# Optimization experiments

Measured on AMD Instinct MI355X. Metric: run time of the kernel, lower is better.

Reference implementation:

```python
import jax, jax.numpy as jnp
import numpy as np

N = 262144
D = 128
E = 524288
N_PHYS = 5
EPS_SL = 1e-8
EPS_LN = 1e-5


def _signed_log(x):
    return jnp.sign(x) * jnp.log(jnp.abs(x) + EPS_SL)


def setup_inputs() -> dict:
    key = jax.random.key(0)
    ks = jax.random.split(key, 12)
    h = jax.random.normal(ks[0], (N, D), dtype=jnp.float32)
    c1 = jax.random.normal(ks[1], (N,), dtype=jnp.float32)
    c2 = jax.random.normal(ks[2], (N,), dtype=jnp.float32)
    c3 = jax.random.normal(ks[3], (N,), dtype=jnp.float32)
    c4 = jax.random.normal(ks[4], (N,), dtype=jnp.float32)
    q_new = jax.random.normal(ks[5], (N,), dtype=jnp.float32)
    src = jax.random.randint(ks[6], (E,), 0, N, dtype=jnp.int64)
    dst = jax.random.randint(ks[7], (E,), 0, N, dtype=jnp.int64)
    d_in = 2 * D + N_PHYS
    W1 = jax.random.normal(ks[8], (d_in, D), dtype=jnp.float32) / np.sqrt(d_in)
    b1 = jnp.zeros((D,), dtype=jnp.float32)
    W2 = jax.random.normal(ks[9], (D, D), dtype=jnp.float32) / np.sqrt(D)
    b2 = jnp.zeros((D,), dtype=jnp.float32)
    gamma = jnp.ones((D,), dtype=jnp.float32)
    beta = jnp.zeros((D,), dtype=jnp.float32)
    return {"h": h, "c1_next_upstream": c1, "c2_prev_upstream": c2,
            "c3_self": c3, "c4_lateral": c4, "q_new": q_new,
            "src": src, "dst": dst,
            "W1": W1, "b1": b1, "W2": W2, "b2": b2,
            "gamma": gamma, "beta": beta}


def reference(h, c1_next_upstream, c2_prev_upstream, c3_self, c4_lateral,
              q_new, src, dst, W1, b1, W2, b2, gamma, beta):
    # sparse adjacency matmul: upstream_h[i] = sum_{j: j->i} h[j]
    upstream_h = jax.ops.segment_sum(h[src], dst, num_segments=h.shape[0])
    phys = jnp.stack([_signed_log(c1_next_upstream),
                      _signed_log(c2_prev_upstream),
                      _signed_log(c3_self),
                      _signed_log(c4_lateral),
                      _signed_log(q_new)], axis=-1)  # (N, 5)
    node_input = jnp.concatenate([h, upstream_h, phys], axis=-1)  # (N, 2D+5)
    hid = jax.nn.silu(node_input @ W1 + b1)
    mlp_out = hid @ W2 + b2
    z = h + mlp_out
    mean = jnp.mean(z, axis=-1, keepdims=True)
    var = jnp.var(z, axis=-1, keepdims=True)
    return (z - mean) * jax.lax.rsqrt(var + EPS_LN) * gamma + beta
```

## Files before the change

kernel.cpp:

```cpp
#include <hip/hip_runtime.h>
#include <math.h>

#define NN 262144
#define DD 128
#define EPS_SL 1e-8f
#define EPS_LN 1e-5f
#define THREADS 512
#define TILE_M 64
#define NBLOCKS 256
#define NTILES (NN / TILE_M)
#define TPB (NTILES / NBLOCKS)

typedef __attribute__((ext_vector_type(8))) short bf16x8;
typedef __attribute__((ext_vector_type(4))) float f32x4;

#define OFF_W1 0
#define OFF_W2 73728
#define OFF_X  106496
#define OFF_H  143360
#define OFF_RED 159744
#define SMEM_TOT 161792

#define WS_OFFS   0
#define WS_CURSOR 1048832
#define WS_BSUM   2097408
#define WS_ESRC   2101504
#define WS_NEEDED (2101504 + 524288 * 4)

__device__ inline unsigned short f2bf(float f) {
    union { float f; unsigned int i; } v; v.f = f;
    unsigned int r = v.i + 0x7fffu + ((v.i >> 16) & 1u);
    return (unsigned short)(r >> 16);
}
__device__ inline unsigned int pack2(float a, float b) {
    return (unsigned int)f2bf(a) | ((unsigned int)f2bf(b) << 16);
}
__device__ inline uint4 pack8(float4 a, float4 b) {
    return make_uint4(pack2(a.x, a.y), pack2(a.z, a.w),
                      pack2(b.x, b.y), pack2(b.z, b.w));
}
__device__ inline float signed_log(float x) {
    float l = __logf(fabsf(x) + EPS_SL);
    return (x > 0.f) ? l : ((x < 0.f) ? -l : 0.f);
}
__device__ inline void stx(unsigned short* sX, int kb, int row, uint4 v) {
    *(uint4*)(sX + (((kb * 64 + row) ^ (kb & 7)) * 8)) = v;
}
__device__ inline bf16x8 ldx(const unsigned short* sX, int kb, int row) {
    return *(const bf16x8*)(sX + (((kb * 64 + row) ^ (kb & 7)) * 8));
}

__global__ void hist_kernel(const int* __restrict__ dst, int* counts, int E) {
    int e = blockIdx.x * blockDim.x + threadIdx.x;
    if (e < E) atomicAdd(&counts[dst[e]], 1);
}

__global__ void scan_local(int* offs, int* bsum) {
    __shared__ int tmp[256];
    int t = threadIdx.x, i = blockIdx.x * 256 + t;
    int own = offs[i];
    tmp[t] = own;
    __syncthreads();
    for (int off = 1; off < 256; off <<= 1) {
        int v = (t >= off) ? tmp[t - off] : 0;
        __syncthreads();
        tmp[t] += v;
        __syncthreads();
    }
    offs[i] = tmp[t] - own;
    if (t == 255) bsum[blockIdx.x] = tmp[255];
}

__global__ void scan_bsum(int* bsum) {
    __shared__ int tmp[1024];
    int t = threadIdx.x;
    int own = bsum[t];
    tmp[t] = own;
    __syncthreads();
    for (int off = 1; off < 1024; off <<= 1) {
        int v = (t >= off) ? tmp[t - off] : 0;
        __syncthreads();
        tmp[t] += v;
        __syncthreads();
    }
    bsum[t] = tmp[t] - own;
}

__global__ void scan_fixup(int* offs, const int* __restrict__ bsum, int* cursor, int E) {
    int i = blockIdx.x * 256 + threadIdx.x;
    int v = offs[i] + bsum[i >> 8];
    offs[i] = v;
    cursor[i] = v;
    if (i == 0) offs[NN] = E;
}

__global__ void fill_kernel(const int* __restrict__ src, const int* __restrict__ dst,
                            int* cursor, int* esrc, int E) {
    int e = blockIdx.x * blockDim.x + threadIdx.x;
    if (e < E) {
        int p = atomicAdd(&cursor[dst[e]], 1);
        esrc[p] = src[e];
    }
}

__global__ __launch_bounds__(256) void gather_kernel(
    const float4* __restrict__ h4, const int* __restrict__ offs,
    const int* __restrict__ esrc, char* outb)
{
    int stride = gridDim.x * 256;
    for (int idx = blockIdx.x * 256 + threadIdx.x; idx < NN * 16; idx += stride) {
        int n = idx >> 4, c = idx & 15;
        int o0 = offs[n], o1 = offs[n + 1];
        float4 a = make_float4(0.f, 0.f, 0.f, 0.f);
        float4 b = make_float4(0.f, 0.f, 0.f, 0.f);
        for (int e = o0; e < o1; ++e) {
            const float4* hr = h4 + (size_t)esrc[e] * 32 + c * 2;
            float4 p0 = hr[0], p1 = hr[1];
            a.x += p0.x; a.y += p0.y; a.z += p0.z; a.w += p0.w;
            b.x += p1.x; b.y += p1.y; b.z += p1.z; b.w += p1.w;
        }
        *(uint4*)(outb + (size_t)n * 512 + c * 16) = pack8(a, b);
    }
}

__global__ void scatter_kernel(const float4* __restrict__ h4,
                               const int* __restrict__ src,
                               const int* __restrict__ dst,
                               float* up, int E) {
    int tid = blockIdx.x * blockDim.x + threadIdx.x;
    int e = tid >> 5;
    if (e >= E) return;
    int c = tid & 31;
    float4 v = h4[(size_t)src[e] * 32 + c];
    float* o = up + (size_t)dst[e] * DD + c * 4;
    atomicAdd(o + 0, v.x);
    atomicAdd(o + 1, v.y);
    atomicAdd(o + 2, v.z);
    atomicAdd(o + 3, v.w);
}

template <int GATHER>
__global__ __launch_bounds__(THREADS) void node_kernel(
    const float* __restrict__ h, const void* up,
    const float* __restrict__ c1, const float* __restrict__ c2,
    const float* __restrict__ c3, const float* __restrict__ c4,
    const float* __restrict__ qn,
    const float* __restrict__ W1, const float* __restrict__ b1,
    const float* __restrict__ W2, const float* __restrict__ b2,
    const float* __restrict__ gamma, const float* __restrict__ beta,
    float* out)
{
    extern __shared__ char smem[];
    unsigned short* sW1 = (unsigned short*)(smem + OFF_W1);
    unsigned short* sW2 = (unsigned short*)(smem + OFF_W2);
    unsigned short* sX  = (unsigned short*)(smem + OFF_X);
    unsigned short* sH  = (unsigned short*)(smem + OFF_H);
    float2* red = (float2*)(smem + OFF_RED);

    const int tid = threadIdx.x;

    for (int c = tid; c < 36 * 128; c += THREADS) {
        int kb = c >> 7, n = c & 127;
        unsigned short tmp[8] __attribute__((aligned(16)));
        #pragma unroll
        for (int j = 0; j < 8; ++j) {
            int k = kb * 8 + j;
            tmp[j] = (k < 261) ? f2bf(W1[k * DD + n]) : (unsigned short)0;
        }
        *(uint4*)(sW1 + c * 8) = *(const uint4*)tmp;
    }
    for (int c = tid; c < 16 * 128; c += THREADS) {
        int kb = c >> 7, n = c & 127;
        unsigned short tmp[8] __attribute__((aligned(16)));
        #pragma unroll
        for (int j = 0; j < 8; ++j) tmp[j] = f2bf(W2[(kb * 8 + j) * DD + n]);
        *(uint4*)(sW2 + c * 8) = *(const uint4*)tmp;
    }
    if (tid < 192) {
        int kb = 33 + (tid >> 6), row = tid & 63;
        stx(sX, kb, row, make_uint4(0u, 0u, 0u, 0u));
    }

    const int lane = tid & 63;
    const int w    = tid >> 6;
    const int wm   = w >> 2;
    const int wn   = w & 3;
    const int l15  = lane & 15;
    const int lk   = lane >> 4;
    const int col0 = wn * 32 + l15;
    const int col1 = col0 + 16;

    const float b1v[2] = {b1[col0], b1[col1]};
    const float b2v[2] = {b2[col0], b2[col1]};
    const float gv[2]  = {gamma[col0], gamma[col1]};
    const float bv[2]  = {beta[col0], beta[col1]};

    const bf16x8* W1f = (const bf16x8*)sW1;
    const bf16x8* Hf  = (const bf16x8*)sH;
    const bf16x8* W2f = (const bf16x8*)sW2;

    const int k0 = tid & 15;
    const int r0 = tid >> 4;

    float4 h0a, h0b, h1a, h1b;
    uint4  u0, u1;
    float4 v0a, v0b, v1a, v1b;
    float pc1 = 0.f, pc2 = 0.f, pc3 = 0.f, pc4 = 0.f, pc5 = 0.f;

    {
        int base = blockIdx.x * TPB * TILE_M;
        const float* hp = h + (size_t)(base + r0) * DD + k0 * 8;
        h0a = *(const float4*)hp;       h0b = *(const float4*)(hp + 4);
        h1a = *(const float4*)(hp + 32 * DD); h1b = *(const float4*)(hp + 32 * DD + 4);
        if (GATHER) {
            const char* ub = (const char*)up;
            u0 = *(const uint4*)(ub + (size_t)(base + r0) * 512 + k0 * 16);
            u1 = *(const uint4*)(ub + (size_t)(base + r0 + 32) * 512 + k0 * 16);
        } else {
            const float* uf = (const float*)up + (size_t)(base + r0) * DD + k0 * 8;
            v0a = *(const float4*)uf;       v0b = *(const float4*)(uf + 4);
            v1a = *(const float4*)(uf + 32 * DD); v1b = *(const float4*)(uf + 32 * DD + 4);
        }
        if (tid < 64) {
            int n0 = base + tid;
            pc1 = c1[n0]; pc2 = c2[n0]; pc3 = c3[n0]; pc4 = c4[n0]; pc5 = qn[n0];
        }
    }
    __syncthreads();

    for (int tt = 0; tt < TPB; ++tt) {
        const int base = (blockIdx.x * TPB + tt) * TILE_M;

        stx(sX, k0, r0,      pack8(h0a, h0b));
        stx(sX, k0, r0 + 32, pack8(h1a, h1b));
        if (GATHER) {
            stx(sX, 16 + k0, r0,      u0);
            stx(sX, 16 + k0, r0 + 32, u1);
        } else {
            stx(sX, 16 + k0, r0,      pack8(v0a, v0b));
            stx(sX, 16 + k0, r0 + 32, pack8(v1a, v1b));
        }
        if (tid < 64) {
            uint4 pv = make_uint4(pack2(signed_log(pc1), signed_log(pc2)),
                                  pack2(signed_log(pc3), signed_log(pc4)),
                                  pack2(signed_log(pc5), 0.f), 0u);
            stx(sX, 32, tid, pv);
        }

        if (tt + 1 < TPB) {
            int bn = base + TILE_M;
            const float* hp = h + (size_t)(bn + r0) * DD + k0 * 8;
            h0a = *(const float4*)hp;       h0b = *(const float4*)(hp + 4);
            h1a = *(const float4*)(hp + 32 * DD); h1b = *(const float4*)(hp + 32 * DD + 4);
            if (GATHER) {
                const char* ub = (const char*)up;
                u0 = *(const uint4*)(ub + (size_t)(bn + r0) * 512 + k0 * 16);
                u1 = *(const uint4*)(ub + (size_t)(bn + r0 + 32) * 512 + k0 * 16);
            } else {
                const float* uf = (const float*)up + (size_t)(bn + r0) * DD + k0 * 8;
                v0a = *(const float4*)uf;       v0b = *(const float4*)(uf + 4);
                v1a = *(const float4*)(uf + 32 * DD); v1b = *(const float4*)(uf + 32 * DD + 4);
            }
            if (tid < 64) {
                int n0 = bn + tid;
                pc1 = c1[n0]; pc2 = c2[n0]; pc3 = c3[n0]; pc4 = c4[n0]; pc5 = qn[n0];
            }
        }
        __syncthreads();

        f32x4 acc[2][2] = {};
        #pragma unroll
        for (int ks = 0; ks < 9; ++ks) {
            int kb = ks * 4 + lk;
            bf16x8 a0  = ldx(sX, kb, wm * 32 + l15);
            bf16x8 a1  = ldx(sX, kb, wm * 32 + 16 + l15);
            bf16x8 bb0 = W1f[kb * 128 + col0];
            bf16x8 bb1 = W1f[kb * 128 + col1];
            acc[0][0] = __builtin_amdgcn_mfma_f32_16x16x32_bf16(a0, bb0, acc[0][0], 0, 0, 0);
            acc[0][1] = __builtin_amdgcn_mfma_f32_16x16x32_bf16(a0, bb1, acc[0][1], 0, 0, 0);
            acc[1][0] = __builtin_amdgcn_mfma_f32_16x16x32_bf16(a1, bb0, acc[1][0], 0, 0, 0);
            acc[1][1] = __builtin_amdgcn_mfma_f32_16x16x32_bf16(a1, bb1, acc[1][1], 0, 0, 0);
        }
        #pragma unroll
        for (int fm = 0; fm < 2; ++fm) {
            int row = wm * 32 + fm * 16 + lk * 4;
            #pragma unroll
            for (int fn = 0; fn < 2; ++fn) {
                int col = wn * 32 + fn * 16 + l15;
                int kbh = col >> 3, ko = col & 7;
                #pragma unroll
                for (int r = 0; r < 4; ++r) {
                    float v = acc[fm][fn][r] + b1v[fn];
                    float sg = 1.f / (1.f + __expf(-v));
                    sH[(kbh * 64 + row + r) * 8 + ko] = f2bf(v * sg);
                }
            }
        }
        __syncthreads();

        f32x4 acc2[2][2] = {};
        #pragma unroll
        for (int ks = 0; ks < 4; ++ks) {
            int kb = ks * 4 + lk;
            bf16x8 a0  = Hf[kb * 64 + wm * 32 + l15];
            bf16x8 a1  = Hf[kb * 64 + wm * 32 + 16 + l15];
            bf16x8 bb0 = W2f[kb * 128 + col0];
            bf16x8 bb1 = W2f[kb * 128 + col1];
            acc2[0][0] = __builtin_amdgcn_mfma_f32_16x16x32_bf16(a0, bb0, acc2[0][0], 0, 0, 0);
            acc2[0][1] = __builtin_amdgcn_mfma_f32_16x16x32_bf16(a0, bb1, acc2[0][1], 0, 0, 0);
            acc2[1][0] = __builtin_amdgcn_mfma_f32_16x16x32_bf16(a1, bb0, acc2[1][0], 0, 0, 0);
            acc2[1][1] = __builtin_amdgcn_mfma_f32_16x16x32_bf16(a1, bb1, acc2[1][1], 0, 0, 0);
        }

        float rs1[2][4], rs2[2][4];
        #pragma unroll
        for (int fm = 0; fm < 2; ++fm) {
            #pragma unroll
            for (int r = 0; r < 4; ++r) {
                size_t rowg = (size_t)(base + wm * 32 + fm * 16 + lk * 4 + r) * DD;
                float z0 = acc2[fm][0][r] + b2v[0] + h[rowg + col0];
                float z1 = acc2[fm][1][r] + b2v[1] + h[rowg + col1];
                acc2[fm][0][r] = z0; acc2[fm][1][r] = z1;
                float s = z0 + z1, q = z0 * z0 + z1 * z1;
                #pragma unroll
                for (int off = 1; off < 16; off <<= 1) {
                    s += __shfl_xor(s, off);
                    q += __shfl_xor(q, off);
                }
                rs1[fm][r] = s; rs2[fm][r] = q;
            }
        }
        if (l15 == 0) {
            #pragma unroll
            for (int fm = 0; fm < 2; ++fm)
                #pragma unroll
                for (int r = 0; r < 4; ++r)
                    red[wn * 64 + wm * 32 + fm * 16 + lk * 4 + r] =
                        make_float2(rs1[fm][r], rs2[fm][r]);
        }
        __syncthreads();

        #pragma unroll
        for (int fm = 0; fm < 2; ++fm) {
            #pragma unroll
            for (int r = 0; r < 4; ++r) {
                int rloc = wm * 32 + fm * 16 + lk * 4 + r;
                float2 t0 = red[rloc], t1 = red[64 + rloc],
                       t2 = red[128 + rloc], t3 = red[192 + rloc];
                float S = t0.x + t1.x + t2.x + t3.x;
                float Q = t0.y + t1.y + t2.y + t3.y;
                float mean = S * (1.f / 128.f);
                float var  = Q * (1.f / 128.f) - mean * mean;
                float rstd = rsqrtf(var + EPS_LN);
                size_t rowg = (size_t)(base + rloc) * DD;
                out[rowg + col0] = (acc2[fm][0][r] - mean) * rstd * gv[0] + bv[0];
                out[rowg + col1] = (acc2[fm][1][r] - mean) * rstd * gv[1] + bv[1];
            }
        }
    }
}

extern "C" void kernel_launch(void* const* d_in, const int* in_sizes, int n_in,
                              void* d_out, int out_size, void* d_ws, size_t ws_size,
                              hipStream_t stream) {
    const float* h     = (const float*)d_in[0];
    const float* c1    = (const float*)d_in[1];
    const float* c2    = (const float*)d_in[2];
    const float* c3    = (const float*)d_in[3];
    const float* c4    = (const float*)d_in[4];
    const float* qn    = (const float*)d_in[5];
    const int*   src   = (const int*)d_in[6];
    const int*   dst   = (const int*)d_in[7];
    const float* W1    = (const float*)d_in[8];
    const float* b1    = (const float*)d_in[9];
    const float* W2    = (const float*)d_in[10];
    const float* b2    = (const float*)d_in[11];
    const float* gamma = (const float*)d_in[12];
    const float* beta  = (const float*)d_in[13];
    float* out = (float*)d_out;
    int E = in_sizes[6];

    if (ws_size >= (size_t)WS_NEEDED) {
        char* ws = (char*)d_ws;
        int* offs   = (int*)(ws + WS_OFFS);
        int* cursor = (int*)(ws + WS_CURSOR);
        int* bsum   = (int*)(ws + WS_BSUM);
        int* esrc   = (int*)(ws + WS_ESRC);

        hipMemsetAsync(offs, 0, (size_t)NN * sizeof(int), stream);
        int eb = (E + 255) / 256;
        hist_kernel<<<eb, 256, 0, stream>>>(dst, offs, E);
        scan_local<<<NN / 256, 256, 0, stream>>>(offs, bsum);
        scan_bsum<<<1, 1024, 0, stream>>>(bsum);
        scan_fixup<<<NN / 256, 256, 0, stream>>>(offs, bsum, cursor, E);
        fill_kernel<<<eb, 256, 0, stream>>>(src, dst, cursor, esrc, E);

        gather_kernel<<<2048, 256, 0, stream>>>((const float4*)h, offs, esrc, (char*)d_out);

        hipFuncSetAttribute(reinterpret_cast<const void*>(&node_kernel<1>),
                            hipFuncAttributeMaxDynamicSharedMemorySize, SMEM_TOT);
        node_kernel<1><<<NBLOCKS, THREADS, SMEM_TOT, stream>>>(
            h, d_out, c1, c2, c3, c4, qn,
            W1, b1, W2, b2, gamma, beta, out);
    } else {
        hipMemsetAsync(d_out, 0, (size_t)NN * DD * sizeof(float), stream);
        int sthreads = E * 32;
        int sblocks = (sthreads + 255) / 256;
        scatter_kernel<<<sblocks, 256, 0, stream>>>((const float4*)h, src, dst, out, E);
        hipFuncSetAttribute(reinterpret_cast<const void*>(&node_kernel<0>),
                            hipFuncAttributeMaxDynamicSharedMemorySize, SMEM_TOT);
        node_kernel<0><<<NBLOCKS, THREADS, SMEM_TOT, stream>>>(
            h, d_out, c1, c2, c3, c4, qn,
            W1, b1, W2, b2, gamma, beta, out);
    }
}
```

Measured before the change: 232.6 us.

## Pack h with gathered sums in bf16 slots and rewrite node kernel per-wave

The gather kernel now also writes h itself as bf16 into the second half of each 512-byte output slot, so the node kernel reads one contiguous bf16 row per node instead of separate fp32 h and upstream buffers. The node kernel is restructured so that each wave independently handles 16-row strips. It uses transposed MFMA operands, a per-wave LDS hidden buffer and shuffle-based LayerNorm, which removes block-wide syncs and the staged X tile. The W1 rows are permuted to match the new slot order. The residual add now uses the bf16-rounded copy of h, which reduces precision slightly.

```diff
diff --git a/kernel.cpp b/kernel.cpp
--- a/kernel.cpp
+++ b/kernel.cpp
@@ -6,32 +6,37 @@
 #define EPS_SL 1e-8f
 #define EPS_LN 1e-5f
 #define THREADS 512
-#define TILE_M 64
 #define NBLOCKS 256
-#define NTILES (NN / TILE_M)
-#define TPB (NTILES / NBLOCKS)
 
 typedef __attribute__((ext_vector_type(8))) short bf16x8;
 typedef __attribute__((ext_vector_type(4))) float f32x4;
 
-#define OFF_W1 0
-#define OFF_W2 73728
-#define OFF_X  106496
-#define OFF_H  143360
-#define OFF_RED 159744
-#define SMEM_TOT 161792
+#define OFF_W1  0
+#define OFF_W2  73728
+#define OFF_B   106496
+#define OFF_HID 108544
+#define SMEM_TOT 141312
+
+#define FB_OFF_W1 0
+#define FB_OFF_W2 73728
+#define FB_OFF_X  106496
+#define FB_OFF_H  143360
+#define FB_OFF_RED 159744
+#define FB_SMEM_TOT 161792
 
 #define WS_OFFS   0
 #define WS_CURSOR 1048832
 #define WS_BSUM   2097408
 #define WS_ESRC   2101504
-#define WS_NEEDED (2101504 + 524288 * 4)
 
 __device__ inline unsigned short f2bf(float f) {
     union { float f; unsigned int i; } v; v.f = f;
     unsigned int r = v.i + 0x7fffu + ((v.i >> 16) & 1u);
     return (unsigned short)(r >> 16);
 }
+__device__ inline float bf2f(unsigned short u) {
+    union { float f; unsigned int i; } v; v.i = ((unsigned int)u) << 16; return v.f;
+}
 __device__ inline unsigned int pack2(float a, float b) {
     return (unsigned int)f2bf(a) | ((unsigned int)f2bf(b) << 16);
 }
@@ -43,10 +48,10 @@
     float l = __logf(fabsf(x) + EPS_SL);
     return (x > 0.f) ? l : ((x < 0.f) ? -l : 0.f);
 }
-__device__ inline void stx(unsigned short* sX, int kb, int row, uint4 v) {
+__device__ inline void stx64(unsigned short* sX, int kb, int row, uint4 v) {
     *(uint4*)(sX + (((kb * 64 + row) ^ (kb & 7)) * 8)) = v;
 }
-__device__ inline bf16x8 ldx(const unsigned short* sX, int kb, int row) {
+__device__ inline bf16x8 ldx64(const unsigned short* sX, int kb, int row) {
     return *(const bf16x8*)(sX + (((kb * 64 + row) ^ (kb & 7)) * 8));
 }
 
@@ -119,7 +124,11 @@
             a.x += p0.x; a.y += p0.y; a.z += p0.z; a.w += p0.w;
             b.x += p1.x; b.y += p1.y; b.z += p1.z; b.w += p1.w;
         }
-        *(uint4*)(outb + (size_t)n * 512 + c * 16) = pack8(a, b);
+        const float4* hn = h4 + (size_t)n * 32 + c * 2;
+        float4 q0 = hn[0], q1 = hn[1];
+        char* slot = outb + (size_t)n * 512;
+        *(uint4*)(slot + c * 16)       = pack8(a, b);
+        *(uint4*)(slot + 256 + c * 16) = pack8(q0, q1);
     }
 }
 
@@ -139,9 +148,8 @@
     atomicAdd(o + 3, v.w);
 }
 
-template <int GATHER>
-__global__ __launch_bounds__(THREADS) void node_kernel(
-    const float* __restrict__ h, const void* up,
+__global__ __launch_bounds__(THREADS, 2) void node_kernel(
+    const void* slots,
     const float* __restrict__ c1, const float* __restrict__ c2,
     const float* __restrict__ c3, const float* __restrict__ c4,
     const float* __restrict__ qn,
@@ -153,19 +161,24 @@
     extern __shared__ char smem[];
     unsigned short* sW1 = (unsigned short*)(smem + OFF_W1);
     unsigned short* sW2 = (unsigned short*)(smem + OFF_W2);
-    unsigned short* sX  = (unsigned short*)(smem + OFF_X);
-    unsigned short* sH  = (unsigned short*)(smem + OFF_H);
-    float2* red = (float2*)(smem + OFF_RED);
-
-    const int tid = threadIdx.x;
+    float* sB = (float*)(smem + OFF_B);
+
+    const int tid  = threadIdx.x;
+    const int lane = tid & 63;
+    const int wv   = tid >> 6;
+    const int m    = lane & 15;
+    const int lk   = lane >> 4;
+    unsigned short* sHid = (unsigned short*)(smem + OFF_HID + wv * 4096);
+    const int hswz = (m & 3) << 5;
 
     for (int c = tid; c < 36 * 128; c += THREADS) {
         int kb = c >> 7, n = c & 127;
         unsigned short tmp[8] __attribute__((aligned(16)));
         #pragma unroll
         for (int j = 0; j < 8; ++j) {
-            int k = kb * 8 + j;
-            tmp[j] = (k < 261) ? f2bf(W1[k * DD + n]) : (unsigned short)0;
+            int kx = kb * 8 + j;
+            int krow = (kx < 128) ? (128 + kx) : (kx < 256 ? kx - 128 : kx);
+            tmp[j] = (krow < 261) ? f2bf(W1[krow * DD + n]) : (unsigned short)0;
         }
         *(uint4*)(sW1 + c * 8) = *(const uint4*)tmp;
     }
@@ -176,9 +189,151 @@
         for (int j = 0; j < 8; ++j) tmp[j] = f2bf(W2[(kb * 8 + j) * DD + n]);
         *(uint4*)(sW2 + c * 8) = *(const uint4*)tmp;
     }
+    if (tid < 128) {
+        sB[tid]       = b1[tid];
+        sB[128 + tid] = b2[tid];
+        sB[256 + tid] = gamma[tid];
+        sB[384 + tid] = beta[tid];
+    }
+    __syncthreads();
+
+    const int strip0 = (blockIdx.x * 8 + wv) * 8;
+
+    for (int it = 0; it < 8; ++it) {
+        const int rbase = (strip0 + it) * 16;
+        const char* slot = (const char*)slots + (size_t)(rbase + m) * 512;
+
+        bf16x8 xa[8];
+        #pragma unroll
+        for (int ks = 0; ks < 8; ++ks)
+            xa[ks] = *(const bf16x8*)(slot + ks * 64 + lk * 16);
+
+        bf16x8 xp = {};
+        if (lane < 16) {
+            int n0 = rbase + m;
+            xp[0] = (short)f2bf(signed_log(c1[n0]));
+            xp[1] = (short)f2bf(signed_log(c2[n0]));
+            xp[2] = (short)f2bf(signed_log(c3[n0]));
+            xp[3] = (short)f2bf(signed_log(c4[n0]));
+            xp[4] = (short)f2bf(signed_log(qn[n0]));
+        }
+
+        uint2 hres[8];
+        #pragma unroll
+        for (int ct = 0; ct < 8; ++ct)
+            hres[ct] = *(const uint2*)(slot + 256 + (ct * 16 + lk * 4) * 2);
+
+        f32x4 acc1[8] = {};
+        #pragma unroll
+        for (int ks = 0; ks < 8; ++ks) {
+            #pragma unroll
+            for (int ct = 0; ct < 8; ++ct) {
+                bf16x8 wf = *(const bf16x8*)(sW1 + (((ks * 4 + lk) * 128) + ct * 16 + m) * 8);
+                acc1[ct] = __builtin_amdgcn_mfma_f32_16x16x32_bf16(wf, xa[ks], acc1[ct], 0, 0, 0);
+            }
+        }
+        #pragma unroll
+        for (int ct = 0; ct < 8; ++ct) {
+            bf16x8 wf = *(const bf16x8*)(sW1 + (((32 + lk) * 128) + ct * 16 + m) * 8);
+            acc1[ct] = __builtin_amdgcn_mfma_f32_16x16x32_bf16(wf, xp, acc1[ct], 0, 0, 0);
+        }
+
+        #pragma unroll
+        for (int ct = 0; ct < 8; ++ct) {
+            float4 b1v = *(const float4*)(sB + ct * 16 + lk * 4);
+            float v0 = acc1[ct][0] + b1v.x, v1 = acc1[ct][1] + b1v.y;
+            float v2 = acc1[ct][2] + b1v.z, v3 = acc1[ct][3] + b1v.w;
+            float s0 = v0 / (1.f + __expf(-v0));
+            float s1 = v1 / (1.f + __expf(-v1));
+            float s2 = v2 / (1.f + __expf(-v2));
+            float s3 = v3 / (1.f + __expf(-v3));
+            char* hb = (char*)sHid + m * 256 + ((ct * 32 + lk * 8) ^ hswz);
+            *(uint2*)hb = make_uint2(pack2(s0, s1), pack2(s2, s3));
+        }
+
+        f32x4 acc2[8] = {};
+        #pragma unroll
+        for (int ks = 0; ks < 4; ++ks) {
+            bf16x8 hbf = *(const bf16x8*)((char*)sHid + m * 256 + ((ks * 64 + lk * 16) ^ hswz));
+            #pragma unroll
+            for (int ct = 0; ct < 8; ++ct) {
+                bf16x8 wf = *(const bf16x8*)(sW2 + (((ks * 4 + lk) * 128) + ct * 16 + m) * 8);
+                acc2[ct] = __builtin_amdgcn_mfma_f32_16x16x32_bf16(wf, hbf, acc2[ct], 0, 0, 0);
+            }
+        }
+
+        float s = 0.f, q = 0.f;
+        #pragma unroll
+        for (int ct = 0; ct < 8; ++ct) {
+            float4 b2v = *(const float4*)(sB + 128 + ct * 16 + lk * 4);
+            float z0 = acc2[ct][0] + b2v.x + bf2f((unsigned short)(hres[ct].x & 0xffff));
+            float z1 = acc2[ct][1] + b2v.y + bf2f((unsigned short)(hres[ct].x >> 16));
+            float z2 = acc2[ct][2] + b2v.z + bf2f((unsigned short)(hres[ct].y & 0xffff));
+            float z3 = acc2[ct][3] + b2v.w + bf2f((unsigned short)(hres[ct].y >> 16));
+            acc2[ct][0] = z0; acc2[ct][1] = z1; acc2[ct][2] = z2; acc2[ct][3] = z3;
+            s += (z0 + z1) + (z2 + z3);
+            q += (z0 * z0 + z1 * z1) + (z2 * z2 + z3 * z3);
+        }
+        s += __shfl_xor(s, 16); q += __shfl_xor(q, 16);
+        s += __shfl_xor(s, 32); q += __shfl_xor(q, 32);
+        float mean = s * (1.f / 128.f);
+        float var  = q * (1.f / 128.f) - mean * mean;
+        float rstd = rsqrtf(var + EPS_LN);
+
+        float* op = out + (size_t)(rbase + m) * DD;
+        #pragma unroll
+        for (int ct = 0; ct < 8; ++ct) {
+            float4 g  = *(const float4*)(sB + 256 + ct * 16 + lk * 4);
+            float4 bt = *(const float4*)(sB + 384 + ct * 16 + lk * 4);
+            float4 o;
+            o.x = (acc2[ct][0] - mean) * rstd * g.x + bt.x;
+            o.y = (acc2[ct][1] - mean) * rstd * g.y + bt.y;
+            o.z = (acc2[ct][2] - mean) * rstd * g.z + bt.z;
+            o.w = (acc2[ct][3] - mean) * rstd * g.w + bt.w;
+            *(float4*)(op + ct * 16 + lk * 4) = o;
+        }
+    }
+}
+
+__global__ __launch_bounds__(512) void node_kernel_fb(
+    const float* __restrict__ h, const float* up,
+    const float* __restrict__ c1, const float* __restrict__ c2,
+    const float* __restrict__ c3, const float* __restrict__ c4,
+    const float* __restrict__ qn,
+    const float* __restrict__ W1, const float* __restrict__ b1,
+    const float* __restrict__ W2, const float* __restrict__ b2,
+    const float* __restrict__ gamma, const float* __restrict__ beta,
+    float* out)
+{
+    extern __shared__ char smem[];
+    unsigned short* sW1 = (unsigned short*)(smem + FB_OFF_W1);
+    unsigned short* sW2 = (unsigned short*)(smem + FB_OFF_W2);
+    unsigned short* sX  = (unsigned short*)(smem + FB_OFF_X);
+    unsigned short* sH  = (unsigned short*)(smem + FB_OFF_H);
+    float2* red = (float2*)(smem + FB_OFF_RED);
+
+    const int tid = threadIdx.x;
+
+    for (int c = tid; c < 36 * 128; c += 512) {
+        int kb = c >> 7, n = c & 127;
+        unsigned short tmp[8] __attribute__((aligned(16)));
+        #pragma unroll
+        for (int j = 0; j < 8; ++j) {
+            int k = kb * 8 + j;
+            tmp[j] = (k < 261) ? f2bf(W1[k * DD + n]) : (unsigned short)0;
+        }
+        *(uint4*)(sW1 + c * 8) = *(const uint4*)tmp;
+    }
+    for (int c = tid; c < 16 * 128; c += 512) {
+        int kb = c >> 7, n = c & 127;
+        unsigned short tmp[8] __attribute__((aligned(16)));
+        #pragma unroll
+        for (int j = 0; j < 8; ++j) tmp[j] = f2bf(W2[(kb * 8 + j) * DD + n]);
+        *(uint4*)(sW2 + c * 8) = *(const uint4*)tmp;
+    }
     if (tid < 192) {
         int kb = 33 + (tid >> 6), row = tid & 63;
-        stx(sX, kb, row, make_uint4(0u, 0u, 0u, 0u));
+        stx64(sX, kb, row, make_uint4(0u, 0u, 0u, 0u));
     }
 
     const int lane = tid & 63;
@@ -202,25 +357,17 @@
     const int k0 = tid & 15;
     const int r0 = tid >> 4;
 
-    float4 h0a, h0b, h1a, h1b;
-    uint4  u0, u1;
-    float4 v0a, v0b, v1a, v1b;
+    float4 h0a, h0b, h1a, h1b, v0a, v0b, v1a, v1b;
     float pc1 = 0.f, pc2 = 0.f, pc3 = 0.f, pc4 = 0.f, pc5 = 0.f;
 
     {
-        int base = blockIdx.x * TPB * TILE_M;
+        int base = blockIdx.x * 16 * 64;
         const float* hp = h + (size_t)(base + r0) * DD + k0 * 8;
-        h0a = *(const float4*)hp;       h0b = *(const float4*)(hp + 4);
+        h0a = *(const float4*)hp;             h0b = *(const float4*)(hp + 4);
         h1a = *(const float4*)(hp + 32 * DD); h1b = *(const float4*)(hp + 32 * DD + 4);
-        if (GATHER) {
-            const char* ub = (const char*)up;
-            u0 = *(const uint4*)(ub + (size_t)(base + r0) * 512 + k0 * 16);
-            u1 = *(const uint4*)(ub + (size_t)(base + r0 + 32) * 512 + k0 * 16);
-        } else {
-            const float* uf = (const float*)up + (size_t)(base + r0) * DD + k0 * 8;
-            v0a = *(const float4*)uf;       v0b = *(const float4*)(uf + 4);
-            v1a = *(const float4*)(uf + 32 * DD); v1b = *(const float4*)(uf + 32 * DD + 4);
-        }
+        const float* uf = up + (size_t)(base + r0) * DD + k0 * 8;
+        v0a = *(const float4*)uf;             v0b = *(const float4*)(uf + 4);
+        v1a = *(const float4*)(uf + 32 * DD); v1b = *(const float4*)(uf + 32 * DD + 4);
         if (tid < 64) {
             int n0 = base + tid;
             pc1 = c1[n0]; pc2 = c2[n0]; pc3 = c3[n0]; pc4 = c4[n0]; pc5 = qn[n0];
@@ -228,39 +375,27 @@
     }
     __syncthreads();
 
-    for (int tt = 0; tt < TPB; ++tt) {
-        const int base = (blockIdx.x * TPB + tt) * TILE_M;
-
-        stx(sX, k0, r0,      pack8(h0a, h0b));
-        stx(sX, k0, r0 + 32, pack8(h1a, h1b));
-        if (GATHER) {
-            stx(sX, 16 + k0, r0,      u0);
-            stx(sX, 16 + k0, r0 + 32, u1);
-        } else {
-            stx(sX, 16 + k0, r0,      pack8(v0a, v0b));
-            stx(sX, 16 + k0, r0 + 32, pack8(v1a, v1b));
-        }
+    for (int tt = 0; tt < 16; ++tt) {
+        const int base = (blockIdx.x * 16 + tt) * 64;
+
+        stx64(sX, k0, r0,           pack8(h0a, h0b));
+        stx64(sX, k0, r0 + 32,      pack8(h1a, h1b));
+        stx64(sX, 16 + k0, r0,      pack8(v0a, v0b));
+        stx64(sX, 16 + k0, r0 + 32, pack8(v1a, v1b));
         if (tid < 64) {
             uint4 pv = make_uint4(pack2(signed_log(pc1), signed_log(pc2)),
                                   pack2(signed_log(pc3), signed_log(pc4)),
                                   pack2(signed_log(pc5), 0.f), 0u);
-            stx(sX, 32, tid, pv);
-        }
-
-        if (tt + 1 < TPB) {
-            int bn = base + TILE_M;
+            stx64(sX, 32, tid, pv);
+        }
+        if (tt + 1 < 16) {
+            int bn = base + 64;
             const float* hp = h + (size_t)(bn + r0) * DD + k0 * 8;
-            h0a = *(const float4*)hp;       h0b = *(const float4*)(hp + 4);
+            h0a = *(const float4*)hp;             h0b = *(const float4*)(hp + 4);
             h1a = *(const float4*)(hp + 32 * DD); h1b = *(const float4*)(hp + 32 * DD + 4);
-            if (GATHER) {
-                const char* ub = (const char*)up;
-                u0 = *(const uint4*)(ub + (size_t)(bn + r0) * 512 + k0 * 16);
-                u1 = *(const uint4*)(ub + (size_t)(bn + r0 + 32) * 512 + k0 * 16);
-            } else {
-                const float* uf = (const float*)up + (size_t)(bn + r0) * DD + k0 * 8;
-                v0a = *(const float4*)uf;       v0b = *(const float4*)(uf + 4);
-                v1a = *(const float4*)(uf + 32 * DD); v1b = *(const float4*)(uf + 32 * DD + 4);
-            }
+            const float* uf = up + (size_t)(bn + r0) * DD + k0 * 8;
+            v0a = *(const float4*)uf;             v0b = *(const float4*)(uf + 4);
+            v1a = *(const float4*)(uf + 32 * DD); v1b = *(const float4*)(uf + 32 * DD + 4);
             if (tid < 64) {
                 int n0 = bn + tid;
                 pc1 = c1[n0]; pc2 = c2[n0]; pc3 = c3[n0]; pc4 = c4[n0]; pc5 = qn[n0];
@@ -272,8 +407,8 @@
         #pragma unroll
         for (int ks = 0; ks < 9; ++ks) {
             int kb = ks * 4 + lk;
-            bf16x8 a0  = ldx(sX, kb, wm * 32 + l15);
-            bf16x8 a1  = ldx(sX, kb, wm * 32 + 16 + l15);
+            bf16x8 a0  = ldx64(sX, kb, wm * 32 + l15);
+            bf16x8 a1  = ldx64(sX, kb, wm * 32 + 16 + l15);
             bf16x8 bb0 = W1f[kb * 128 + col0];
             bf16x8 bb1 = W1f[kb * 128 + col1];
             acc[0][0] = __builtin_amdgcn_mfma_f32_16x16x32_bf16(a0, bb0, acc[0][0], 0, 0, 0);
@@ -379,8 +514,9 @@
     const float* beta  = (const float*)d_in[13];
     float* out = (float*)d_out;
     int E = in_sizes[6];
-
-    if (ws_size >= (size_t)WS_NEEDED) {
+    size_t ws_needed = (size_t)WS_ESRC + (size_t)E * 4;
+
+    if (ws_size >= ws_needed) {
         char* ws = (char*)d_ws;
         int* offs   = (int*)(ws + WS_OFFS);
         int* cursor = (int*)(ws + WS_CURSOR);
@@ -397,20 +533,20 @@
 
         gather_kernel<<<2048, 256, 0, stream>>>((const float4*)h, offs, esrc, (char*)d_out);
 
-        hipFuncSetAttribute(reinterpret_cast<const void*>(&node_kernel<1>),
+        hipFuncSetAttribute(reinterpret_cast<const void*>(&node_kernel),
                             hipFuncAttributeMaxDynamicSharedMemorySize, SMEM_TOT);
-        node_kernel<1><<<NBLOCKS, THREADS, SMEM_TOT, stream>>>(
-            h, d_out, c1, c2, c3, c4, qn,
+        node_kernel<<<NBLOCKS, THREADS, SMEM_TOT, stream>>>(
+            d_out, c1, c2, c3, c4, qn,
             W1, b1, W2, b2, gamma, beta, out);
     } else {
         hipMemsetAsync(d_out, 0, (size_t)NN * DD * sizeof(float), stream);
         int sthreads = E * 32;
         int sblocks = (sthreads + 255) / 256;
         scatter_kernel<<<sblocks, 256, 0, stream>>>((const float4*)h, src, dst, out, E);
-        hipFuncSetAttribute(reinterpret_cast<const void*>(&node_kernel<0>),
-                            hipFuncAttributeMaxDynamicSharedMemorySize, SMEM_TOT);
-        node_kernel<0><<<NBLOCKS, THREADS, SMEM_TOT, stream>>>(
-            h, d_out, c1, c2, c3, c4, qn,
+        hipFuncSetAttribute(reinterpret_cast<const void*>(&node_kernel_fb),
+                            hipFuncAttributeMaxDynamicSharedMemorySize, FB_SMEM_TOT);
+        node_kernel_fb<<<256, 512, FB_SMEM_TOT, stream>>>(
+            h, out, c1, c2, c3, c4, qn,
             W1, b1, W2, b2, gamma, beta, out);
     }
 }
```

Result: slower. 252.2 us (+8.4%).
